# Kernel optimization log

Measured on AMD Instinct MI355X. Metric: run time of the kernel, lower is better.

The kernel has to match this reference:

```python
import jax, jax.numpy as jnp
import numpy as np

EPS_LN = 1e-5
EPS_BN = 1e-5


def ln_channels(x, w, b):
    # LayerNorm2d: normalize over channel dim of NCHW
    mu = x.mean(axis=1, keepdims=True)
    var = x.var(axis=1, keepdims=True)
    return (x - mu) / jnp.sqrt(var + EPS_LN) * w[None, :, None, None] + b[None, :, None, None]


def bn_eval(x, g, b):
    # eval-mode BatchNorm2d with running_mean=0, running_var=1
    return x / jnp.sqrt(1.0 + EPS_BN) * g[None, :, None, None] + b[None, :, None, None]


def conv1x1(x, w, b):
    return jnp.einsum('bchw,oc->bohw', x, w) + b[None, :, None, None]


def q_shift(x):
    # directional shift: 4 channel quarters shifted right/left/down/up by 1 px (zero pad)
    C = x.shape[1]
    q = C // 4
    return jnp.concatenate([
        jnp.pad(x[:, 0 * q:1 * q, :, :-1], ((0, 0), (0, 0), (0, 0), (1, 0))),
        jnp.pad(x[:, 1 * q:2 * q, :, 1:], ((0, 0), (0, 0), (0, 0), (0, 1))),
        jnp.pad(x[:, 2 * q:3 * q, :-1, :], ((0, 0), (0, 0), (1, 0), (0, 0))),
        jnp.pad(x[:, 3 * q:4 * q, 1:, :], ((0, 0), (0, 0), (0, 1), (0, 0))),
    ], axis=1)


def wkv_scan(k, v, w_neg, u):
    # numerically-stable RWKV WKV recurrence. k, v: [N, T, C]; w_neg (negative decay), u: [C]
    N, T, C = k.shape

    def step(carry, kv):
        a, b, p = carry
        kt, vt = kv
        q = jnp.maximum(p, u + kt)
        e1 = jnp.exp(p - q)
        e2 = jnp.exp(u + kt - q)
        out = (e1 * a + e2 * vt) / (e1 * b + e2)
        q2 = jnp.maximum(p + w_neg, kt)
        f1 = jnp.exp(p + w_neg - q2)
        f2 = jnp.exp(kt - q2)
        return (f1 * a + f2 * vt, f1 * b + f2, q2), out

    init = (jnp.zeros((N, C), k.dtype), jnp.zeros((N, C), k.dtype), jnp.full((N, C), -1e38, k.dtype))
    _, outs = jax.lax.scan(step, init, (jnp.swapaxes(k, 0, 1), jnp.swapaxes(v, 0, 1)))
    return jnp.swapaxes(outs, 0, 1)


def shape_guided_rwkv(x, mask, mix_k, mix_v, mix_r, Wk, Wv, Wr, Wo, decay, first, kn_w, kn_b):
    B, C, H, W = x.shape
    xs = q_shift(x)
    x_sh = mask * xs + (1.0 - mask) * x  # saliency-guided shift blend
    mk = mix_k[None, :, None, None]
    mv = mix_v[None, :, None, None]
    mr = mix_r[None, :, None, None]
    xk = x * mk + x_sh * (1.0 - mk)
    xv = x * mv + x_sh * (1.0 - mv)
    xr = x * mr + x_sh * (1.0 - mr)
    k = jnp.einsum('bchw,oc->bohw', xk, Wk)
    v = jnp.einsum('bchw,oc->bohw', xv, Wv)
    sr = jax.nn.sigmoid(jnp.einsum('bchw,oc->bohw', xr, Wr))
    w_neg = -jnp.exp(decay)
    # horizontal orientation: scan each row left->right
    kh = k.transpose(0, 2, 3, 1).reshape(B * H, W, C)
    vh = v.transpose(0, 2, 3, 1).reshape(B * H, W, C)
    wkv_h = wkv_scan(kh, vh, w_neg, first).reshape(B, H, W, C).transpose(0, 3, 1, 2)
    # vertical orientation: scan each column top->bottom
    kv_ = k.transpose(0, 3, 2, 1).reshape(B * W, H, C)
    vv_ = v.transpose(0, 3, 2, 1).reshape(B * W, H, C)
    wkv_v = wkv_scan(kv_, vv_, w_neg, first).reshape(B, W, H, C).transpose(0, 3, 2, 1)
    wkv = 0.5 * (wkv_h + wkv_v)
    wkv = ln_channels(wkv, kn_w, kn_b)  # key_norm=True
    out = jnp.einsum('bchw,oc->bohw', sr * wkv, Wo)
    return x + out


def channel_fusion(x, c1_w, c1_b, bn1_g, bn1_b, c2_w, c2_b, bn2_g, bn2_b, c3_w, c3_b, bn3_g, bn3_b):
    # grouped 3x3 conv (groups=2) -> GELU -> BN -> 1x1 expand -> GELU -> BN -> 1x1 reduce -> GELU -> BN
    y = jax.lax.conv_general_dilated(x, c1_w, (1, 1), 'SAME',
                                     dimension_numbers=('NCHW', 'OIHW', 'NCHW'),
                                     feature_group_count=2) + c1_b[None, :, None, None]
    y = bn_eval(jax.nn.gelu(y, approximate=False), bn1_g, bn1_b)
    y = bn_eval(jax.nn.gelu(conv1x1(y, c2_w, c2_b), approximate=False), bn2_g, bn2_b)
    y = bn_eval(jax.nn.gelu(conv1x1(y, c3_w, c3_b), approximate=False), bn3_g, bn3_b)
    return y


def patch_expand(x, up_w, up_b, s=2):
    B, C, H, W = x.shape
    y = conv1x1(x, up_w, up_b)  # [B, Cout*s*s, H, W]
    Cout = y.shape[1] // (s * s)
    y = y.reshape(B, Cout, s, s, H, W).transpose(0, 1, 4, 2, 5, 3).reshape(B, Cout, H * s, W * s)
    return y


def setup_inputs() -> dict:
    key = jax.random.key(0)
    B, C, Cs, Cout, H, W, s = 8, 256, 512, 128, 64, 64, 2
    ks = jax.random.split(key, 32)
    sc = C ** -0.5
    inp = {
        'x': jax.random.normal(ks[0], (B, C, H, W), jnp.float32),
        'skip': jax.random.normal(ks[1], (B, Cs, H, W), jnp.float32),
        'saliency_mask': jax.random.uniform(ks[2], (B, 1, H, W), jnp.float32),
        'ln1_w': jnp.ones((C,)), 'ln1_b': jnp.zeros((C,)),
        'ln2_w': jnp.ones((C,)), 'ln2_b': jnp.zeros((C,)),
        'mix_k': jax.random.uniform(ks[3], (C,)),
        'mix_v': jax.random.uniform(ks[4], (C,)),
        'mix_r': jax.random.uniform(ks[5], (C,)),
        'Wk': jax.random.normal(ks[6], (C, C)) * sc,
        'Wv': jax.random.normal(ks[7], (C, C)) * sc,
        'Wr': jax.random.normal(ks[8], (C, C)) * sc,
        'Wo': jax.random.normal(ks[9], (C, C)) * sc,
        'decay': jax.random.normal(ks[10], (C,)) * 0.5,
        'first': jax.random.normal(ks[11], (C,)) * 0.5,
        'kn_w': jnp.ones((C,)), 'kn_b': jnp.zeros((C,)),
        'sp_w': jax.random.normal(ks[12], (C, Cs)) * (Cs ** -0.5),
        'sp_b': jnp.zeros((C,)),
        'c1_w': jax.random.normal(ks[13], (2 * C, C, 3, 3)) * ((C * 9) ** -0.5),
        'c1_b': jnp.zeros((2 * C,)),
        'bn1_g': jnp.ones((2 * C,)), 'bn1_b': jnp.zeros((2 * C,)),
        'c2_w': jax.random.normal(ks[14], (4 * C, 2 * C)) * ((2 * C) ** -0.5),
        'c2_b': jnp.zeros((4 * C,)),
        'bn2_g': jnp.ones((4 * C,)), 'bn2_b': jnp.zeros((4 * C,)),
        'c3_w': jax.random.normal(ks[15], (C, 4 * C)) * ((4 * C) ** -0.5),
        'c3_b': jnp.zeros((C,)),
        'bn3_g': jnp.ones((C,)), 'bn3_b': jnp.zeros((C,)),
        'up_w': jax.random.normal(ks[16], (Cout * s * s, C)) * sc,
        'up_b': jnp.zeros((Cout * s * s,)),
    }
    return inp


def reference(x, skip, saliency_mask, ln1_w, ln1_b, ln2_w, ln2_b, mix_k, mix_v, mix_r,
              Wk, Wv, Wr, Wo, decay, first, kn_w, kn_b, sp_w, sp_b,
              c1_w, c1_b, bn1_g, bn1_b, c2_w, c2_b, bn2_g, bn2_b, c3_w, c3_b, bn3_g, bn3_b,
              up_w, up_b):
    xn = ln_channels(x, ln1_w, ln1_b)
    x_sg = shape_guided_rwkv(xn, saliency_mask, mix_k, mix_v, mix_r, Wk, Wv, Wr, Wo,
                             decay, first, kn_w, kn_b)
    skip_feat = conv1x1(skip, sp_w, sp_b)
    x_cat = jnp.concatenate([x_sg, skip_feat], axis=1)
    x_fused = channel_fusion(x_cat, c1_w, c1_b, bn1_g, bn1_b, c2_w, c2_b, bn2_g, bn2_b,
                             c3_w, c3_b, bn3_g, bn3_b)
    x_fused = ln_channels(x_fused, ln2_w, ln2_b)
    return patch_expand(x_fused, up_w, up_b, s=2)
```

## Files before the change

### kernel.cpp

```cpp
#include <hip/hip_runtime.h>
#include <hip/hip_bf16.h>
#include <math.h>

#define B_ 8
#define C_ 256
#define P_ 4096

typedef __bf16 bf16_t;
typedef __attribute__((ext_vector_type(8))) __bf16 bf16x8;
typedef __attribute__((ext_vector_type(4))) float f32x4;

template<typename T>
__global__ __launch_bounds__(256)
void ln_stats_kernel(const T* __restrict__ in, float2* __restrict__ stats)
{
    __shared__ float sred[4][64];
    __shared__ float s2red[4][64];
    int tid = threadIdx.x;
    int wp = tid & 63, cw = tid >> 6;
    int gp = blockIdx.x * 64 + wp;
    int b  = gp >> 12, p = gp & 4095;
    size_t base = (size_t)b * 256 * 4096 + p;
    float s = 0.f, s2 = 0.f;
    #pragma unroll 8
    for (int cc = 0; cc < 64; ++cc) {
        float v = (float)in[base + (size_t)(cw * 64 + cc) * 4096];
        s += v; s2 += v * v;
    }
    sred[cw][wp] = s; s2red[cw][wp] = s2;
    __syncthreads();
    if (cw == 0) {
        s  = sred[0][wp]  + sred[1][wp]  + sred[2][wp]  + sred[3][wp];
        s2 = s2red[0][wp] + s2red[1][wp] + s2red[2][wp] + s2red[3][wp];
        float mu  = s * (1.f / 256.f);
        float var = s2 * (1.f / 256.f) - mu * mu;
        stats[gp] = make_float2(mu, 1.0f / sqrtf(var + 1e-5f));
    }
}

__global__ __launch_bounds__(256)
void qshift_mix_kernel(const float* __restrict__ x, const float2* __restrict__ st1,
                       const float* __restrict__ mask,
                       const float* __restrict__ gw, const float* __restrict__ gb,
                       const float* __restrict__ mk_, const float* __restrict__ mv_,
                       const float* __restrict__ mr_,
                       bf16_t* __restrict__ xk, bf16_t* __restrict__ xv,
                       bf16_t* __restrict__ xr)
{
    int g = blockIdx.x * 256 + threadIdx.x;
    int p = g & 4095;
    int c = (g >> 12) & 255;
    int b = g >> 20;
    int h = p >> 6, w = p & 63;
    float gwc = gw[c], gbc = gb[c];
    float2 stc = st1[(b << 12) + p];
    float xcv = (x[g] - stc.x) * stc.y * gwc + gbc;
    float xs = 0.f;
    int quad = c >> 6;
    int d = 0; bool ok = false;
    if (quad == 0)      { ok = (w > 0);  d = -1;  }
    else if (quad == 1) { ok = (w < 63); d = 1;   }
    else if (quad == 2) { ok = (h > 0);  d = -64; }
    else                { ok = (h < 63); d = 64;  }
    if (ok) {
        float2 st2 = st1[(b << 12) + p + d];
        xs = (x[g + d] - st2.x) * st2.y * gwc + gbc;
    }
    float m = mask[(b << 12) + p];
    float xsh = m * xs + (1.f - m) * xcv;
    float a;
    a = mk_[c]; xk[g] = (bf16_t)(a * xcv + (1.f - a) * xsh);
    a = mv_[c]; xv[g] = (bf16_t)(a * xcv + (1.f - a) * xsh);
    a = mr_[c]; xr[g] = (bf16_t)(a * xcv + (1.f - a) * xsh);
}

#define EP_NONE    0
#define EP_SIGMOID 1
#define EP_BIAS    2
#define EP_RESLN   3
#define EP_GELU_BN 4
#define EP_SHUFFLE 5
#define EP_KVR     6
#define EP_WOSKIP  7

template<int NB, int BMODE, int EPI, int OUTBF>
__global__ __launch_bounds__(256, 2)
void mfma_gemm(const bf16_t* __restrict__ Wp, const void* __restrict__ Xin,
               const bf16_t* __restrict__ X2,
               const float2* __restrict__ bstats, const float* __restrict__ blnw,
               const float* __restrict__ blnb,
               const float* __restrict__ bias, const float* __restrict__ skipin,
               const float* __restrict__ bng, const float* __restrict__ bnb,
               const float* __restrict__ resx, const float2* __restrict__ estats,
               const float* __restrict__ elnw, const float* __restrict__ elnb,
               void* __restrict__ OutV,
               int O, int K, int Cstride, int obs, int ocoff)
{
    constexpr int BROWS = (NB == 3) ? 2 * 66 : 128;
    __shared__ bf16_t Alds[NB * 128 * 36];
    __shared__ bf16_t Blds[BROWS * 36];
    int tid = threadIdx.x;
    int bx = blockIdx.x;
    int o0 = blockIdx.y * 128;
    int b  = blockIdx.z;
    int p0 = bx << 7;
    int cbase = (NB == 3) ? ((o0 >> 8) << 8) : 0;

    bool wo = true;
    int bb = b;
    if (EPI == EP_WOSKIP) { wo = (b >> 3) == 0; bb = b & 7; }

    const bf16_t* Wpe = Wp;
    if (EPI == EP_KVR)    Wpe = Wp + (size_t)(b >> 3) * O * K;
    if (EPI == EP_WOSKIP) Wpe = wo ? Wp : (Wp + 65536);
    int Krun = K;
    if (EPI == EP_WOSKIP) Krun = wo ? 256 : 512;

    int lane = tid & 63, wid = tid >> 6;
    int l15 = lane & 15;
    int lk8 = (lane >> 4) << 3;
    int mbase = (wid >> 1) << 6;
    int nbase = (wid & 1) << 6;

    const bf16_t* Xb_bf = (const bf16_t*)Xin + (size_t)bb * Cstride * 4096;
    const float*  Xb_f  = (const float*)Xin + (size_t)bb * Cstride * 4096;
    const bf16_t* X2b   = (BMODE == 3) ? X2 + (size_t)bb * Cstride * 4096 : nullptr;
    const float*  skf   = (EPI == EP_WOSKIP)
                          ? skipin + (size_t)bb * 512 * 4096 : nullptr;

    f32x4 acc[4][4] = {};

    if (NB == 3 && tid < 144) {
        int r = tid / 72, rest = tid % 72;
        int col = rest / 36, cc = rest % 36;
        Blds[(r * 66 + (col ? 65 : 0)) * 36 + cc] = (bf16_t)0.f;
    }

    for (int kh = 0; kh < NB; ++kh) {
        for (int c0 = 0; c0 < Krun; c0 += 32) {
            __syncthreads();
            if (NB == 3) {
                int wpos = tid & 63, cgr = tid >> 6;
                #pragma unroll
                for (int r = 0; r < 2; ++r) {
                    int hr = (bx << 1) + kh - 1 + r;
                    bf16x8 bv;
                    #pragma unroll
                    for (int i = 0; i < 8; ++i) bv[i] = (bf16_t)0.f;
                    if (hr >= 0 && hr < 64) {
                        size_t gb = (size_t)(cbase + c0 + cgr * 8) * 4096 + (hr << 6) + wpos;
                        #pragma unroll
                        for (int j = 0; j < 8; ++j) bv[j] = Xb_bf[gb + (size_t)j * 4096];
                    }
                    *reinterpret_cast<bf16x8*>(&Blds[(r * 66 + wpos + 1) * 36 + cgr * 8]) = bv;
                }
            } else {
                #pragma unroll
                for (int rep = 0; rep < 2; ++rep) {
                    int p_loc = tid & 127;
                    int cgr = (tid >> 7) + rep * 2;
                    bf16x8 bv;
                    size_t gbase = (size_t)(c0 + cgr * 8) * 4096 + p0 + p_loc;
                    float2 st = make_float2(0.f, 1.f);
                    if (BMODE >= 2 && (EPI != EP_WOSKIP || wo))
                        st = bstats[(bb << 12) + p0 + p_loc];
                    #pragma unroll
                    for (int j = 0; j < 8; ++j) {
                        size_t gi = gbase + (size_t)j * 4096;
                        int cc = c0 + cgr * 8 + j;
                        if (EPI == EP_WOSKIP && !wo) {
                            bv[j] = (bf16_t)skf[gi];
                        } else if (BMODE == 0) {
                            bv[j] = Xb_bf[gi];
                        } else if (BMODE == 1) {
                            bv[j] = (bf16_t)Xb_f[gi];
                        } else {
                            float v = ((float)Xb_bf[gi] - st.x) * st.y * blnw[cc] + blnb[cc];
                            if (BMODE == 3) v *= (float)X2b[gi];
                            bv[j] = (bf16_t)v;
                        }
                    }
                    *reinterpret_cast<bf16x8*>(&Blds[p_loc * 36 + cgr * 8]) = bv;
                }
            }
            {
                int ao = tid >> 1, aq = tid & 1;
                #pragma unroll
                for (int t = 0; t < NB; ++t) {
                    const bf16_t* wsrc = (NB == 3)
                        ? Wpe + ((size_t)(kh * 3 + t) * O + o0 + ao) * 256 + c0
                        : Wpe + (size_t)(o0 + ao) * Krun + c0;
                    bf16x8 w0 = *reinterpret_cast<const bf16x8*>(wsrc + aq * 8);
                    bf16x8 w1 = *reinterpret_cast<const bf16x8*>(wsrc + (aq + 2) * 8);
                    *reinterpret_cast<bf16x8*>(&Alds[(t * 128 + ao) * 36 + aq * 8]) = w0;
                    *reinterpret_cast<bf16x8*>(&Alds[(t * 128 + ao) * 36 + (aq + 2) * 8]) = w1;
                }
            }
            __syncthreads();
            #pragma unroll
            for (int t = 0; t < NB; ++t) {
                bf16x8 af[4];
                #pragma unroll
                for (int i = 0; i < 4; ++i)
                    af[i] = *reinterpret_cast<const bf16x8*>(
                              &Alds[(t * 128 + mbase + i * 16 + l15) * 36 + lk8]);
                #pragma unroll
                for (int j = 0; j < 4; ++j) {
                    int pl = nbase + j * 16;
                    int baddr;
                    if (NB == 3)
                        baddr = ((pl >> 6) * 66 + (pl & 63) + l15 + t) * 36 + lk8;
                    else
                        baddr = (pl + l15) * 36 + lk8;
                    bf16x8 bfv = *reinterpret_cast<const bf16x8*>(&Blds[baddr]);
                    #pragma unroll
                    for (int i = 0; i < 4; ++i)
                        acc[i][j] = __builtin_amdgcn_mfma_f32_16x16x32_bf16(
                                        af[i], bfv, acc[i][j], 0, 0, 0);
                }
            }
        }
    }

    const float bnsc = 1.0f / sqrtf(1.f + 1e-5f);
    bool kvr_sig = (EPI == EP_KVR) && (b >= 16);
    int oco = ocoff;
    if (EPI == EP_WOSKIP) oco = wo ? 0 : 256;
    #pragma unroll
    for (int i = 0; i < 4; ++i) {
        #pragma unroll
        for (int r = 0; r < 4; ++r) {
            int o = o0 + mbase + i * 16 + ((lane >> 4) << 2) + r;
            float bi = 0.f;
            if (EPI == EP_BIAS || EPI == EP_GELU_BN || EPI == EP_SHUFFLE) bi = bias[o];
            if (EPI == EP_WOSKIP && !wo) bi = bias[o];
            float sc = 0.f, sh = 0.f;
            if (EPI == EP_GELU_BN) { sc = bng[o] * bnsc; sh = bnb[o]; }
            float rw = 0.f, rb = 0.f;
            if ((EPI == EP_RESLN) || (EPI == EP_WOSKIP && wo)) {
                rw = elnw[o]; rb = elnb[o];
            }
            #pragma unroll
            for (int j = 0; j < 4; ++j) {
                int pp = p0 + nbase + j * 16 + l15;
                float t = acc[i][j][r];
                if (EPI == EP_SIGMOID) t = 1.f / (1.f + expf(-t));
                if (EPI == EP_KVR && kvr_sig) t = 1.f / (1.f + expf(-t));
                if (EPI == EP_BIAS || EPI == EP_GELU_BN || EPI == EP_SHUFFLE) t += bi;
                if (EPI == EP_WOSKIP && !wo) t += bi;
                if ((EPI == EP_RESLN) || (EPI == EP_WOSKIP && wo)) {
                    float2 st = estats[(bb << 12) + pp];
                    float rv = resx[((size_t)bb * 256 + o) * 4096 + pp];
                    t += (rv - st.x) * st.y * rw + rb;
                }
                if (EPI == EP_GELU_BN) {
                    t = 0.5f * t * (1.f + erff(t * 0.70710678118654752f));
                    t = t * sc + sh;
                }
                if (EPI == EP_SHUFFLE) {
                    int co = o >> 2, s1 = (o >> 1) & 1, s2 = o & 1;
                    int hh = pp >> 6, ww = pp & 63;
                    ((float*)OutV)[(((size_t)bb * 128 + co) * 128 + hh * 2 + s1) * 128
                                   + ww * 2 + s2] = t;
                } else {
                    size_t oidx = ((size_t)bb * obs + oco + o) * 4096 + pp;
                    if (OUTBF) ((bf16_t*)OutV)[oidx] = (bf16_t)t;
                    else       ((float*)OutV)[oidx]  = t;
                }
            }
        }
    }
}

__global__ __launch_bounds__(256)
void pack_all_kernel(const float* __restrict__ wk, const float* __restrict__ wv,
                     const float* __restrict__ wr, const float* __restrict__ wo,
                     const float* __restrict__ sp, const float* __restrict__ c2,
                     const float* __restrict__ c3, const float* __restrict__ up,
                     const float* __restrict__ c1, bf16_t* __restrict__ outfl,
                     bf16_t* __restrict__ outc1)
{
    int g = blockIdx.x * 256 + threadIdx.x;
    if (g < 1310720) {
        float v;
        if      (g < 65536)   v = wk[g];
        else if (g < 131072)  v = wv[g - 65536];
        else if (g < 196608)  v = wr[g - 131072];
        else if (g < 262144)  v = wo[g - 196608];
        else if (g < 393216)  v = sp[g - 262144];
        else if (g < 917504)  v = c2[g - 393216];
        else if (g < 1179648) v = c3[g - 917504];
        else                  v = up[g - 1179648];
        outfl[g] = (bf16_t)v;
    } else {
        int g2 = g - 1310720;
        if (g2 < 1179648) {
            int c = g2 & 255;
            int o = (g2 >> 8) & 511;
            int tap = g2 >> 17;
            outc1[g2] = (bf16_t)c1[(size_t)o * 2304 + c * 9 + tap];
        }
    }
}

__global__ __launch_bounds__(64)
void wkv_h_kernel(const bf16_t* __restrict__ kin, const bf16_t* __restrict__ vin,
                  bf16_t* __restrict__ outw,
                  const float* __restrict__ decay, const float* __restrict__ first)
{
    __shared__ bf16_t ks[64 * 66];
    __shared__ bf16_t vs[64 * 66];
    int c0 = blockIdx.x * 64;
    int h  = blockIdx.y;
    int b  = blockIdx.z;
    int tid = threadIdx.x;
    size_t base = (((size_t)b * 256 + c0) * 64 + h) * 64;

    for (int f = tid; f < 64 * 64; f += 64) {
        int cc = f >> 6, w = f & 63;
        ks[cc * 66 + w] = kin[base + (size_t)cc * 4096 + w];
        vs[cc * 66 + w] = vin[base + (size_t)cc * 4096 + w];
    }
    __syncthreads();

    int c = c0 + tid;
    float u  = first[c];
    float wn = -expf(decay[c]);
    float a = 0.f, bb = 0.f, pp = -1e38f;
    for (int t = 0; t < 64; ++t) {
        float kt = (float)ks[tid * 66 + t], vt = (float)vs[tid * 66 + t];
        float q  = fmaxf(pp, u + kt);
        float e1 = expf(pp - q), e2 = expf(u + kt - q);
        float ov = (e1 * a + e2 * vt) / (e1 * bb + e2);
        ks[tid * 66 + t] = (bf16_t)ov;
        float q2 = fmaxf(pp + wn, kt);
        float f1 = expf(pp + wn - q2), f2 = expf(kt - q2);
        a = f1 * a + f2 * vt;
        bb = f1 * bb + f2;
        pp = q2;
    }
    __syncthreads();
    for (int f = tid; f < 64 * 64; f += 64) {
        int cc = f >> 6, w = f & 63;
        outw[base + (size_t)cc * 4096 + w] = ks[cc * 66 + w];
    }
}

__global__ __launch_bounds__(256)
void wkv_v_kernel(const bf16_t* __restrict__ kin, const bf16_t* __restrict__ vin,
                  bf16_t* __restrict__ outw,
                  const float* __restrict__ decay, const float* __restrict__ first)
{
    int g = blockIdx.x * 256 + threadIdx.x;
    int w = g & 63;
    int c = (g >> 6) & 255;
    int b = g >> 14;
    size_t base = (size_t)(b * 256 + c) * 4096 + w;
    float u  = first[c];
    float wn = -expf(decay[c]);
    float a = 0.f, bb = 0.f, pp = -1e38f;
    for (int h = 0; h < 64; ++h) {
        size_t idx = base + h * 64;
        float kt = (float)kin[idx], vt = (float)vin[idx];
        float q  = fmaxf(pp, u + kt);
        float e1 = expf(pp - q), e2 = expf(u + kt - q);
        float ov = (e1 * a + e2 * vt) / (e1 * bb + e2);
        outw[idx] = (bf16_t)(0.5f * ((float)outw[idx] + ov));
        float q2 = fmaxf(pp + wn, kt);
        float f1 = expf(pp + wn - q2), f2 = expf(kt - q2);
        a = f1 * a + f2 * vt;
        bb = f1 * bb + f2;
        pp = q2;
    }
}

extern "C" void kernel_launch(void* const* d_in, const int* in_sizes, int n_in,
                              void* d_out, int out_size, void* d_ws, size_t ws_size,
                              hipStream_t stream)
{
    const float* x      = (const float*)d_in[0];
    const float* skip   = (const float*)d_in[1];
    const float* mask   = (const float*)d_in[2];
    const float* ln1_w  = (const float*)d_in[3];
    const float* ln1_b  = (const float*)d_in[4];
    const float* ln2_w  = (const float*)d_in[5];
    const float* ln2_b  = (const float*)d_in[6];
    const float* mix_k  = (const float*)d_in[7];
    const float* mix_v  = (const float*)d_in[8];
    const float* mix_r  = (const float*)d_in[9];
    const float* Wk     = (const float*)d_in[10];
    const float* Wv     = (const float*)d_in[11];
    const float* Wr     = (const float*)d_in[12];
    const float* Wo     = (const float*)d_in[13];
    const float* decay  = (const float*)d_in[14];
    const float* first  = (const float*)d_in[15];
    const float* kn_w   = (const float*)d_in[16];
    const float* kn_b   = (const float*)d_in[17];
    const float* sp_w   = (const float*)d_in[18];
    const float* sp_b   = (const float*)d_in[19];
    const float* c1_w   = (const float*)d_in[20];
    const float* c1_b   = (const float*)d_in[21];
    const float* bn1_g  = (const float*)d_in[22];
    const float* bn1_b  = (const float*)d_in[23];
    const float* c2_w   = (const float*)d_in[24];
    const float* c2_b   = (const float*)d_in[25];
    const float* bn2_g  = (const float*)d_in[26];
    const float* bn2_b  = (const float*)d_in[27];
    const float* c3_w   = (const float*)d_in[28];
    const float* c3_b   = (const float*)d_in[29];
    const float* bn3_g  = (const float*)d_in[30];
    const float* bn3_b  = (const float*)d_in[31];
    const float* up_w   = (const float*)d_in[32];
    const float* up_b   = (const float*)d_in[33];
    float* out = (float*)d_out;

    float* ws = (float*)d_ws;
    const size_t S = 8388608;
    const size_t Hs = S / 2;
    bf16_t* xk   = (bf16_t*)ws;
    bf16_t* xv   = (bf16_t*)(ws + Hs);
    bf16_t* xr   = (bf16_t*)(ws + 2 * Hs);
    bf16_t* kbuf = (bf16_t*)(ws + 3 * Hs);
    bf16_t* vbuf = (bf16_t*)(ws + 4 * Hs);
    bf16_t* rbuf = (bf16_t*)(ws + 5 * Hs);
    bf16_t* wkv  = (bf16_t*)(ws + 6 * Hs);
    bf16_t* xcat = (bf16_t*)(ws + 7 * Hs);
    bf16_t* y1   = (bf16_t*)(ws + 9 * Hs);
    bf16_t* y2   = (bf16_t*)ws;
    bf16_t* y3   = (bf16_t*)(ws + 4 * Hs);
    float*  wtop = ws + 11 * Hs;
    bf16_t* w9   = (bf16_t*)wtop;
    bf16_t* wfl  = w9 + 1179648;
    float2* st1  = (float2*)(wfl + 1310720);
    float2* stk  = st1 + 32768;
    float2* st2  = stk + 32768;
    bf16_t* wkb = wfl;
    bf16_t* wob = wfl + 196608;
    bf16_t* c2b = wfl + 393216;
    bf16_t* c3b = wfl + 917504;
    bf16_t* upb = wfl + 1179648;

    dim3 blk(256);

    pack_all_kernel<<<dim3(9728), blk, 0, stream>>>(Wk, Wv, Wr, Wo, sp_w, c2_w,
                                                    c3_w, up_w, c1_w, wfl, w9);
    ln_stats_kernel<float><<<dim3(512), blk, 0, stream>>>(x, st1);

    qshift_mix_kernel<<<dim3(32768), blk, 0, stream>>>(x, st1, mask, ln1_w, ln1_b,
                                                       mix_k, mix_v, mix_r, xk, xv, xr);
    mfma_gemm<1, 0, EP_KVR, 1><<<dim3(32, 2, 24), blk, 0, stream>>>(
        wkb, xk, nullptr, nullptr, nullptr, nullptr, nullptr, nullptr, nullptr,
        nullptr, nullptr, nullptr, nullptr, nullptr, kbuf, 256, 256, 256, 256, 0);
    wkv_h_kernel<<<dim3(4, 64, 8), dim3(64), 0, stream>>>(kbuf, vbuf, wkv, decay, first);
    wkv_v_kernel<<<dim3(512), blk, 0, stream>>>(kbuf, vbuf, wkv, decay, first);
    ln_stats_kernel<bf16_t><<<dim3(512), blk, 0, stream>>>(wkv, stk);
    mfma_gemm<1, 3, EP_WOSKIP, 1><<<dim3(32, 2, 16), blk, 0, stream>>>(
        wob, wkv, rbuf, stk, kn_w, kn_b, sp_b, skip, nullptr, nullptr,
        x, st1, ln1_w, ln1_b, xcat, 256, 0, 256, 512, 0);
    mfma_gemm<3, 0, EP_GELU_BN, 1><<<dim3(32, 4, 8), blk, 0, stream>>>(
        w9, xcat, nullptr, nullptr, nullptr, nullptr, c1_b, nullptr, bn1_g, bn1_b,
        nullptr, nullptr, nullptr, nullptr, y1, 512, 256, 512, 512, 0);
    mfma_gemm<1, 0, EP_GELU_BN, 1><<<dim3(32, 8, 8), blk, 0, stream>>>(
        c2b, y1, nullptr, nullptr, nullptr, nullptr, c2_b, nullptr, bn2_g, bn2_b,
        nullptr, nullptr, nullptr, nullptr, y2, 1024, 512, 512, 1024, 0);
    mfma_gemm<1, 0, EP_GELU_BN, 1><<<dim3(32, 2, 8), blk, 0, stream>>>(
        c3b, y2, nullptr, nullptr, nullptr, nullptr, c3_b, nullptr, bn3_g, bn3_b,
        nullptr, nullptr, nullptr, nullptr, y3, 256, 1024, 1024, 256, 0);
    ln_stats_kernel<bf16_t><<<dim3(512), blk, 0, stream>>>(y3, st2);
    mfma_gemm<1, 2, EP_SHUFFLE, 0><<<dim3(32, 4, 8), blk, 0, stream>>>(
        upb, y3, nullptr, st2, ln2_w, ln2_b, up_b, nullptr, nullptr, nullptr,
        nullptr, nullptr, nullptr, nullptr, out, 512, 256, 256, 0, 0);
}
```

Measured before the change: 507.5 us.

## Vectorize qshift-mix and add 64-wide GEMM tiles for small-output GEMMs

The q-shift/mix kernel now has each thread handle 8 consecutive pixels. It uses float4 loads and bf16x8 stores, and horizontal shifts are resolved in registers, so fewer global loads and stores are issued. The GEMM kernel gains a TILE template parameter, and a 64x64 tile variant with higher occupancy is used for the smaller-output GEMMs (KVR, Wo/skip, c3, upsample), launching more blocks to fill the CUs. The Wo/skip block ordering is also swapped so the longer skip-projection blocks are scheduled first. The risks are lower weight reuse per block and the correctness of the new 64-tile load paths.

```diff
diff --git a/kernel.cpp b/kernel.cpp
--- a/kernel.cpp
+++ b/kernel.cpp
@@ -47,31 +47,87 @@
                        bf16_t* __restrict__ xk, bf16_t* __restrict__ xv,
                        bf16_t* __restrict__ xr)
 {
-    int g = blockIdx.x * 256 + threadIdx.x;
+    int gid = blockIdx.x * 256 + threadIdx.x;
+    int g = gid << 3;
     int p = g & 4095;
     int c = (g >> 12) & 255;
     int b = g >> 20;
-    int h = p >> 6, w = p & 63;
+    int h = p >> 6, w0 = p & 63;
     float gwc = gw[c], gbc = gb[c];
-    float2 stc = st1[(b << 12) + p];
-    float xcv = (x[g] - stc.x) * stc.y * gwc + gbc;
-    float xs = 0.f;
+    int sbase = (b << 12) + p;
+
+    float4 x0 = *reinterpret_cast<const float4*>(&x[g]);
+    float4 x1 = *reinterpret_cast<const float4*>(&x[g + 4]);
+    float xv8[8] = {x0.x, x0.y, x0.z, x0.w, x1.x, x1.y, x1.z, x1.w};
+    float2 s8[8];
+    #pragma unroll
+    for (int i = 0; i < 4; ++i) {
+        float4 t = *reinterpret_cast<const float4*>(&st1[sbase + i * 2]);
+        s8[2 * i]     = make_float2(t.x, t.y);
+        s8[2 * i + 1] = make_float2(t.z, t.w);
+    }
+    float xn8[8];
+    #pragma unroll
+    for (int i = 0; i < 8; ++i)
+        xn8[i] = (xv8[i] - s8[i].x) * s8[i].y * gwc + gbc;
+
+    float xs8[8];
     int quad = c >> 6;
-    int d = 0; bool ok = false;
-    if (quad == 0)      { ok = (w > 0);  d = -1;  }
-    else if (quad == 1) { ok = (w < 63); d = 1;   }
-    else if (quad == 2) { ok = (h > 0);  d = -64; }
-    else                { ok = (h < 63); d = 64;  }
-    if (ok) {
-        float2 st2 = st1[(b << 12) + p + d];
-        xs = (x[g + d] - st2.x) * st2.y * gwc + gbc;
-    }
-    float m = mask[(b << 12) + p];
-    float xsh = m * xs + (1.f - m) * xcv;
-    float a;
-    a = mk_[c]; xk[g] = (bf16_t)(a * xcv + (1.f - a) * xsh);
-    a = mv_[c]; xv[g] = (bf16_t)(a * xcv + (1.f - a) * xsh);
-    a = mr_[c]; xr[g] = (bf16_t)(a * xcv + (1.f - a) * xsh);
+    if (quad == 0) {
+        xs8[0] = 0.f;
+        if (w0 > 0) {
+            float xm = x[g - 1]; float2 sm = st1[sbase - 1];
+            xs8[0] = (xm - sm.x) * sm.y * gwc + gbc;
+        }
+        #pragma unroll
+        for (int i = 1; i < 8; ++i) xs8[i] = xn8[i - 1];
+    } else if (quad == 1) {
+        #pragma unroll
+        for (int i = 0; i < 7; ++i) xs8[i] = xn8[i + 1];
+        xs8[7] = 0.f;
+        if (w0 + 8 < 64) {
+            float xp = x[g + 8]; float2 sp = st1[sbase + 8];
+            xs8[7] = (xp - sp.x) * sp.y * gwc + gbc;
+        }
+    } else {
+        int d = (quad == 2) ? -64 : 64;
+        bool ok = (quad == 2) ? (h > 0) : (h < 63);
+        if (ok) {
+            float4 y0 = *reinterpret_cast<const float4*>(&x[g + d]);
+            float4 y1 = *reinterpret_cast<const float4*>(&x[g + d + 4]);
+            float yv8[8] = {y0.x, y0.y, y0.z, y0.w, y1.x, y1.y, y1.z, y1.w};
+            #pragma unroll
+            for (int i = 0; i < 4; ++i) {
+                float4 t = *reinterpret_cast<const float4*>(&st1[sbase + d + i * 2]);
+                float2 sa = make_float2(t.x, t.y), sb = make_float2(t.z, t.w);
+                xs8[2 * i]     = (yv8[2 * i]     - sa.x) * sa.y * gwc + gbc;
+                xs8[2 * i + 1] = (yv8[2 * i + 1] - sb.x) * sb.y * gwc + gbc;
+            }
+        } else {
+            #pragma unroll
+            for (int i = 0; i < 8; ++i) xs8[i] = 0.f;
+        }
+    }
+
+    float4 m0 = *reinterpret_cast<const float4*>(&mask[sbase]);
+    float4 m1 = *reinterpret_cast<const float4*>(&mask[sbase + 4]);
+    float mm[8] = {m0.x, m0.y, m0.z, m0.w, m1.x, m1.y, m1.z, m1.w};
+    float xsh8[8];
+    #pragma unroll
+    for (int i = 0; i < 8; ++i)
+        xsh8[i] = mm[i] * xs8[i] + (1.f - mm[i]) * xn8[i];
+
+    float ak = mk_[c], av = mv_[c], ar = mr_[c];
+    bf16x8 ok_, ov_, or_;
+    #pragma unroll
+    for (int i = 0; i < 8; ++i) {
+        ok_[i] = (bf16_t)(ak * xn8[i] + (1.f - ak) * xsh8[i]);
+        ov_[i] = (bf16_t)(av * xn8[i] + (1.f - av) * xsh8[i]);
+        or_[i] = (bf16_t)(ar * xn8[i] + (1.f - ar) * xsh8[i]);
+    }
+    *reinterpret_cast<bf16x8*>(&xk[g]) = ok_;
+    *reinterpret_cast<bf16x8*>(&xv[g]) = ov_;
+    *reinterpret_cast<bf16x8*>(&xr[g]) = or_;
 }
 
 #define EP_NONE    0
@@ -83,8 +139,8 @@
 #define EP_KVR     6
 #define EP_WOSKIP  7
 
-template<int NB, int BMODE, int EPI, int OUTBF>
-__global__ __launch_bounds__(256, 2)
+template<int NB, int BMODE, int EPI, int OUTBF, int TILE>
+__global__ __launch_bounds__(256, (TILE == 64) ? 4 : 2)
 void mfma_gemm(const bf16_t* __restrict__ Wp, const void* __restrict__ Xin,
                const bf16_t* __restrict__ X2,
                const float2* __restrict__ bstats, const float* __restrict__ blnw,
@@ -96,19 +152,20 @@
                void* __restrict__ OutV,
                int O, int K, int Cstride, int obs, int ocoff)
 {
-    constexpr int BROWS = (NB == 3) ? 2 * 66 : 128;
-    __shared__ bf16_t Alds[NB * 128 * 36];
+    constexpr int MI = TILE / 32;
+    constexpr int BROWS = (NB == 3) ? 2 * 66 : TILE;
+    __shared__ bf16_t Alds[NB * TILE * 36];
     __shared__ bf16_t Blds[BROWS * 36];
     int tid = threadIdx.x;
     int bx = blockIdx.x;
-    int o0 = blockIdx.y * 128;
+    int o0 = blockIdx.y * TILE;
     int b  = blockIdx.z;
-    int p0 = bx << 7;
+    int p0 = bx * TILE;
     int cbase = (NB == 3) ? ((o0 >> 8) << 8) : 0;
 
     bool wo = true;
     int bb = b;
-    if (EPI == EP_WOSKIP) { wo = (b >> 3) == 0; bb = b & 7; }
+    if (EPI == EP_WOSKIP) { wo = (b >> 3) != 0; bb = b & 7; }
 
     const bf16_t* Wpe = Wp;
     if (EPI == EP_KVR)    Wpe = Wp + (size_t)(b >> 3) * O * K;
@@ -119,8 +176,8 @@
     int lane = tid & 63, wid = tid >> 6;
     int l15 = lane & 15;
     int lk8 = (lane >> 4) << 3;
-    int mbase = (wid >> 1) << 6;
-    int nbase = (wid & 1) << 6;
+    int mbase = (wid >> 1) * (TILE / 2);
+    int nbase = (wid & 1) * (TILE / 2);
 
     const bf16_t* Xb_bf = (const bf16_t*)Xin + (size_t)bb * Cstride * 4096;
     const float*  Xb_f  = (const float*)Xin + (size_t)bb * Cstride * 4096;
@@ -128,7 +185,7 @@
     const float*  skf   = (EPI == EP_WOSKIP)
                           ? skipin + (size_t)bb * 512 * 4096 : nullptr;
 
-    f32x4 acc[4][4] = {};
+    f32x4 acc[MI][MI] = {};
 
     if (NB == 3 && tid < 144) {
         int r = tid / 72, rest = tid % 72;
@@ -155,15 +212,15 @@
                     *reinterpret_cast<bf16x8*>(&Blds[(r * 66 + wpos + 1) * 36 + cgr * 8]) = bv;
                 }
             } else {
+                int p_loc = tid & (TILE - 1);
+                float2 st = make_float2(0.f, 1.f);
+                if (BMODE >= 2 && (EPI != EP_WOSKIP || wo))
+                    st = bstats[(bb << 12) + p0 + p_loc];
                 #pragma unroll
-                for (int rep = 0; rep < 2; ++rep) {
-                    int p_loc = tid & 127;
-                    int cgr = (tid >> 7) + rep * 2;
+                for (int rep = 0; rep < (TILE == 128 ? 2 : 1); ++rep) {
+                    int cgr = (TILE == 128) ? ((tid >> 7) + rep * 2) : (tid >> 6);
                     bf16x8 bv;
                     size_t gbase = (size_t)(c0 + cgr * 8) * 4096 + p0 + p_loc;
-                    float2 st = make_float2(0.f, 1.f);
-                    if (BMODE >= 2 && (EPI != EP_WOSKIP || wo))
-                        st = bstats[(bb << 12) + p0 + p_loc];
                     #pragma unroll
                     for (int j = 0; j < 8; ++j) {
                         size_t gi = gbase + (size_t)j * 4096;
@@ -183,7 +240,7 @@
                     *reinterpret_cast<bf16x8*>(&Blds[p_loc * 36 + cgr * 8]) = bv;
                 }
             }
-            {
+            if (TILE == 128) {
                 int ao = tid >> 1, aq = tid & 1;
                 #pragma unroll
                 for (int t = 0; t < NB; ++t) {
@@ -195,17 +252,22 @@
                     *reinterpret_cast<bf16x8*>(&Alds[(t * 128 + ao) * 36 + aq * 8]) = w0;
                     *reinterpret_cast<bf16x8*>(&Alds[(t * 128 + ao) * 36 + (aq + 2) * 8]) = w1;
                 }
+            } else {
+                int ao = tid >> 2, aq = tid & 3;
+                const bf16_t* wsrc = Wpe + (size_t)(o0 + ao) * Krun + c0;
+                bf16x8 w0 = *reinterpret_cast<const bf16x8*>(wsrc + aq * 8);
+                *reinterpret_cast<bf16x8*>(&Alds[ao * 36 + aq * 8]) = w0;
             }
             __syncthreads();
             #pragma unroll
             for (int t = 0; t < NB; ++t) {
-                bf16x8 af[4];
+                bf16x8 af[MI];
                 #pragma unroll
-                for (int i = 0; i < 4; ++i)
+                for (int i = 0; i < MI; ++i)
                     af[i] = *reinterpret_cast<const bf16x8*>(
-                              &Alds[(t * 128 + mbase + i * 16 + l15) * 36 + lk8]);
+                              &Alds[(t * TILE + mbase + i * 16 + l15) * 36 + lk8]);
                 #pragma unroll
-                for (int j = 0; j < 4; ++j) {
+                for (int j = 0; j < MI; ++j) {
                     int pl = nbase + j * 16;
                     int baddr;
                     if (NB == 3)
@@ -214,7 +276,7 @@
                         baddr = (pl + l15) * 36 + lk8;
                     bf16x8 bfv = *reinterpret_cast<const bf16x8*>(&Blds[baddr]);
                     #pragma unroll
-                    for (int i = 0; i < 4; ++i)
+                    for (int i = 0; i < MI; ++i)
                         acc[i][j] = __builtin_amdgcn_mfma_f32_16x16x32_bf16(
                                         af[i], bfv, acc[i][j], 0, 0, 0);
                 }
@@ -227,7 +289,7 @@
     int oco = ocoff;
     if (EPI == EP_WOSKIP) oco = wo ? 0 : 256;
     #pragma unroll
-    for (int i = 0; i < 4; ++i) {
+    for (int i = 0; i < MI; ++i) {
         #pragma unroll
         for (int r = 0; r < 4; ++r) {
             int o = o0 + mbase + i * 16 + ((lane >> 4) << 2) + r;
@@ -241,7 +303,7 @@
                 rw = elnw[o]; rb = elnb[o];
             }
             #pragma unroll
-            for (int j = 0; j < 4; ++j) {
+            for (int j = 0; j < MI; ++j) {
                 int pp = p0 + nbase + j * 16 + l15;
                 float t = acc[i][j][r];
                 if (EPI == EP_SIGMOID) t = 1.f / (1.f + expf(-t));
@@ -446,28 +508,28 @@
                                                     c3_w, up_w, c1_w, wfl, w9);
     ln_stats_kernel<float><<<dim3(512), blk, 0, stream>>>(x, st1);
 
-    qshift_mix_kernel<<<dim3(32768), blk, 0, stream>>>(x, st1, mask, ln1_w, ln1_b,
-                                                       mix_k, mix_v, mix_r, xk, xv, xr);
-    mfma_gemm<1, 0, EP_KVR, 1><<<dim3(32, 2, 24), blk, 0, stream>>>(
+    qshift_mix_kernel<<<dim3(4096), blk, 0, stream>>>(x, st1, mask, ln1_w, ln1_b,
+                                                      mix_k, mix_v, mix_r, xk, xv, xr);
+    mfma_gemm<1, 0, EP_KVR, 1, 64><<<dim3(64, 4, 24), blk, 0, stream>>>(
         wkb, xk, nullptr, nullptr, nullptr, nullptr, nullptr, nullptr, nullptr,
         nullptr, nullptr, nullptr, nullptr, nullptr, kbuf, 256, 256, 256, 256, 0);
     wkv_h_kernel<<<dim3(4, 64, 8), dim3(64), 0, stream>>>(kbuf, vbuf, wkv, decay, first);
     wkv_v_kernel<<<dim3(512), blk, 0, stream>>>(kbuf, vbuf, wkv, decay, first);
     ln_stats_kernel<bf16_t><<<dim3(512), blk, 0, stream>>>(wkv, stk);
-    mfma_gemm<1, 3, EP_WOSKIP, 1><<<dim3(32, 2, 16), blk, 0, stream>>>(
+    mfma_gemm<1, 3, EP_WOSKIP, 1, 64><<<dim3(64, 4, 16), blk, 0, stream>>>(
         wob, wkv, rbuf, stk, kn_w, kn_b, sp_b, skip, nullptr, nullptr,
         x, st1, ln1_w, ln1_b, xcat, 256, 0, 256, 512, 0);
-    mfma_gemm<3, 0, EP_GELU_BN, 1><<<dim3(32, 4, 8), blk, 0, stream>>>(
+    mfma_gemm<3, 0, EP_GELU_BN, 1, 128><<<dim3(32, 4, 8), blk, 0, stream>>>(
         w9, xcat, nullptr, nullptr, nullptr, nullptr, c1_b, nullptr, bn1_g, bn1_b,
         nullptr, nullptr, nullptr, nullptr, y1, 512, 256, 512, 512, 0);
-    mfma_gemm<1, 0, EP_GELU_BN, 1><<<dim3(32, 8, 8), blk, 0, stream>>>(
+    mfma_gemm<1, 0, EP_GELU_BN, 1, 128><<<dim3(32, 8, 8), blk, 0, stream>>>(
         c2b, y1, nullptr, nullptr, nullptr, nullptr, c2_b, nullptr, bn2_g, bn2_b,
         nullptr, nullptr, nullptr, nullptr, y2, 1024, 512, 512, 1024, 0);
-    mfma_gemm<1, 0, EP_GELU_BN, 1><<<dim3(32, 2, 8), blk, 0, stream>>>(
+    mfma_gemm<1, 0, EP_GELU_BN, 1, 64><<<dim3(64, 4, 8), blk, 0, stream>>>(
         c3b, y2, nullptr, nullptr, nullptr, nullptr, c3_b, nullptr, bn3_g, bn3_b,
         nullptr, nullptr, nullptr, nullptr, y3, 256, 1024, 1024, 256, 0);
     ln_stats_kernel<bf16_t><<<dim3(512), blk, 0, stream>>>(y3, st2);
-    mfma_gemm<1, 2, EP_SHUFFLE, 0><<<dim3(32, 4, 8), blk, 0, stream>>>(
+    mfma_gemm<1, 2, EP_SHUFFLE, 0, 64><<<dim3(64, 8, 8), blk, 0, stream>>>(
         upb, y3, nullptr, st2, ln2_w, ln2_b, up_b, nullptr, nullptr, nullptr,
         nullptr, nullptr, nullptr, nullptr, out, 512, 256, 256, 0, 0);
 }
```

Measured after the change: 479.0 us. 1.06x faster.
